# Optimization experiments

Measured on AMD Instinct MI355X. Metric: run time of the kernel, lower is better.

The kernel has to match this reference:

```python
import jax, jax.numpy as jnp
import numpy as np

B, S, HID = 2, 2048, 4096
NH, NKV, HD = 32, 8, 128
MAX_POS = 4096
SCALE = HD ** -0.5


def _rope_tables():
    inv_freq = 1.0 / (10000.0 ** (np.arange(0, HD, 2, dtype=np.float32) / HD))
    t = np.arange(MAX_POS, dtype=np.float32)
    freqs = np.outer(t, inv_freq)              # [MAX_POS, HD/2]
    emb = np.concatenate([freqs, freqs], axis=-1)  # [MAX_POS, HD]
    return jnp.asarray(np.cos(emb)), jnp.asarray(np.sin(emb))


def setup_inputs() -> dict:
    key = jax.random.key(0)
    ks = jax.random.split(key, 6)
    hidden_states = jax.random.normal(ks[0], (B, S, HID), dtype=jnp.float32)
    position_ids = jnp.broadcast_to(jnp.arange(S, dtype=jnp.int64 if jax.config.jax_enable_x64 else jnp.int32), (B, S))
    cos_table, sin_table = _rope_tables()
    # weights stored [in, out] for x @ W
    sd = HID ** -0.5
    Wq = jax.random.normal(ks[1], (HID, NH * HD), dtype=jnp.float32) * sd
    Wk = jax.random.normal(ks[2], (HID, NKV * HD), dtype=jnp.float32) * sd
    Wv = jax.random.normal(ks[3], (HID, NKV * HD), dtype=jnp.float32) * sd
    Wo = jax.random.normal(ks[4], (NH * HD, HID), dtype=jnp.float32) * sd
    return {"hidden_states": hidden_states, "position_ids": position_ids,
            "cos_table": cos_table, "sin_table": sin_table,
            "Wq": Wq, "Wk": Wk, "Wv": Wv, "Wo": Wo}


def _rotate_half(x):
    x1, x2 = jnp.split(x, 2, axis=-1)
    return jnp.concatenate([-x2, x1], axis=-1)


def reference(hidden_states, position_ids, cos_table, sin_table, Wq, Wk, Wv, Wo):
    b, s, _ = hidden_states.shape
    q = (hidden_states @ Wq).reshape(b, s, NH, HD)
    k = (hidden_states @ Wk).reshape(b, s, NKV, HD)
    v = (hidden_states @ Wv).reshape(b, s, NKV, HD)

    # RoPE, cos/sin gathered by position and unsqueezed at head dim (dim=2, bsnd)
    cos = cos_table[position_ids][:, :, None, :]  # [b, s, 1, hd]
    sin = sin_table[position_ids][:, :, None, :]
    q = q * cos + _rotate_half(q) * sin
    k = k * cos + _rotate_half(k) * sin

    # GQA: expand kv heads to match query heads
    rep = NH // NKV
    k = jnp.repeat(k, rep, axis=2)  # [b, s, NH, hd]
    v = jnp.repeat(v, rep, axis=2)

    scores = jnp.einsum('bqnd,bknd->bnqk', q, k) * SCALE  # [b, NH, s, s]
    causal = jnp.tril(jnp.ones((s, s), dtype=bool))
    scores = jnp.where(causal, scores, jnp.finfo(scores.dtype).min)
    probs = jax.nn.softmax(scores, axis=-1)
    attn = jnp.einsum('bnqk,bknd->bqnd', probs, v)  # [b, s, NH, hd]
    attn = attn.reshape(b, s, NH * HD)
    return attn @ Wo
```

## Files before the change

### kernel.cpp

```cpp
#include <hip/hip_runtime.h>
#include <stdint.h>

typedef unsigned short u16;
typedef __bf16 bf16x8 __attribute__((ext_vector_type(8)));
typedef unsigned short u16x8 __attribute__((ext_vector_type(8)));
typedef unsigned short u16x4 __attribute__((ext_vector_type(4)));
typedef float f32x4 __attribute__((ext_vector_type(4)));

#define B_ 2
#define S_ 2048
#define HID_ 4096
#define NH_ 32
#define NKV_ 8
#define HD_ 128
#define NTOT_ 6144
#define SCALE_ 0.08838834764831845f

#define GLD16(gp, lp)                                                     \
  __builtin_amdgcn_global_load_lds(                                       \
      (__attribute__((address_space(1))) void*)(gp),                      \
      (__attribute__((address_space(3))) void*)(lp), 16, 0, 0)

#define BAR __builtin_amdgcn_s_barrier()
#define PRIO1 __builtin_amdgcn_s_setprio(1)
#define PRIO0 __builtin_amdgcn_s_setprio(0)
#define VM8 asm volatile("s_waitcnt vmcnt(8)" ::: "memory")
#define VM0 asm volatile("s_waitcnt vmcnt(0)" ::: "memory")

__device__ __forceinline__ u16 f2b(float f) {
  union { float f; uint32_t u; } v; v.f = f;
  uint32_t u = v.u;
  u = u + 0x7fffu + ((u >> 16) & 1u);
  return (u16)(u >> 16);
}
__device__ __forceinline__ float b2f(u16 s) {
  union { uint32_t u; float f; } v; v.u = ((uint32_t)s) << 16;
  return v.f;
}
__device__ __forceinline__ bf16x8 ldb8(const u16* p) {
  u16x8 u = *(const u16x8*)p;
  return __builtin_bit_cast(bf16x8, u);
}
__device__ __forceinline__ bf16x8 ldb8b(const char* p) {
  u16x8 u = *(const u16x8*)p;
  return __builtin_bit_cast(bf16x8, u);
}

__global__ __launch_bounds__(256) void k_convx(const float* __restrict__ src,
                                               u16* __restrict__ dst, int n4) {
  int i = blockIdx.x * 256 + threadIdx.x;
  if (i >= n4) return;
  const float4 v = ((const float4*)src)[i];
  u16x4 o = { f2b(v.x), f2b(v.y), f2b(v.z), f2b(v.w) };
  *(u16x4*)(dst + (size_t)i * 4) = o;
}

__global__ __launch_bounds__(256) void k_convT(const float* __restrict__ src,
                                               u16* __restrict__ dst, int N, int Kd) {
  __shared__ u16 tile[64][65];
  int k0 = blockIdx.x * 64, n0 = blockIdx.y * 64;
  int t = threadIdx.x;
  int rr = t >> 4;
  int cc = (t & 15) * 4;
#pragma unroll
  for (int p = 0; p < 4; ++p) {
    int r = p * 16 + rr;
    float4 v = *(const float4*)&src[(size_t)(k0 + r) * N + n0 + cc];
    tile[cc + 0][r] = f2b(v.x);
    tile[cc + 1][r] = f2b(v.y);
    tile[cc + 2][r] = f2b(v.z);
    tile[cc + 3][r] = f2b(v.w);
  }
  __syncthreads();
#pragma unroll
  for (int p = 0; p < 4; ++p) {
    int n = p * 16 + rr;
    u16x4 o = { tile[n][cc], tile[n][cc + 1], tile[n][cc + 2], tile[n][cc + 3] };
    *(u16x4*)&dst[(size_t)(n0 + n) * Kd + k0 + cc] = o;
  }
}

__global__ __launch_bounds__(256) void k_convqkv(const float* __restrict__ Wq,
                                                 const float* __restrict__ Wk,
                                                 const float* __restrict__ Wv,
                                                 u16* __restrict__ dst) {
  __shared__ u16 tile[64][65];
  const int Kd = HID_;
  int k0 = blockIdx.x * 64;
  int ng = blockIdx.y * 64;
  const float* src;
  int N, ns;
  if (ng < 4096)      { src = Wq; N = 4096; ns = ng; }
  else if (ng < 5120) { src = Wk; N = 1024; ns = ng - 4096; }
  else                { src = Wv; N = 1024; ns = ng - 5120; }
  int t = threadIdx.x;
  int rr = t >> 4;
  int cc = (t & 15) * 4;
#pragma unroll
  for (int p = 0; p < 4; ++p) {
    int r = p * 16 + rr;
    float4 v = *(const float4*)&src[(size_t)(k0 + r) * N + ns + cc];
    tile[cc + 0][r] = f2b(v.x);
    tile[cc + 1][r] = f2b(v.y);
    tile[cc + 2][r] = f2b(v.z);
    tile[cc + 3][r] = f2b(v.w);
  }
  __syncthreads();
#pragma unroll
  for (int p = 0; p < 4; ++p) {
    int n = p * 16 + rr;
    u16x4 o = { tile[n][cc], tile[n][cc + 1], tile[n][cc + 2], tile[n][cc + 3] };
    *(u16x4*)&dst[(size_t)(ng + n) * Kd + k0 + cc] = o;
  }
}

__global__ __launch_bounds__(512) void k_gemm_out(const u16* __restrict__ A,
                                                  const u16* __restrict__ Bt,
                                                  float* __restrict__ Cf,
                                                  int M, int N, int Kd) {
  __shared__ __align__(16) char smem[131072];
  const int NT = Kd >> 6;

  int nwg = gridDim.x * gridDim.y;
  int orig = blockIdx.y * gridDim.x + blockIdx.x;
  int cpx = nwg >> 3;
  int swz = (orig & 7) * cpx + (orig >> 3);
  int bx = swz % gridDim.x, by = swz / gridDim.x;
  int m0 = by * 256, n0 = bx * 256;

  int t = threadIdx.x, lane = t & 63, wave = t >> 6;
  int wr = wave >> 2, wc = wave & 3;
  int lg = lane >> 4, l16 = lane & 15;
  int loff = l16 * 64 + ((lg ^ ((l16 >> 1) & 3)) << 4);
  int srow = lane >> 2, schk = (lane & 3) ^ ((lane >> 3) & 3);

  const u16* Asrc = A  + (size_t)(m0 + wave * 32 + srow) * Kd + schk * 8;
  const u16* Bsrc = Bt + (size_t)(n0 + wave * 32 + srow) * Kd + schk * 8;

  f32x4 acc[8][4] = {};

#define OST_A(tile, kc, BB) do {                                              \
    char* d_ = smem + (BB) + ((kc) << 14) + (wave << 11);                     \
    const u16* s_ = Asrc + (size_t)(tile) * 64 + (kc) * 32;                   \
    GLD16(s_, d_); GLD16(s_ + (size_t)16 * Kd, d_ + 1024); } while (0)
#define OST_B(tile, kc, BB) do {                                              \
    char* d_ = smem + (BB) + 32768 + ((kc) << 14) + (wave << 11);             \
    const u16* s_ = Bsrc + (size_t)(tile) * 64 + (kc) * 32;                   \
    GLD16(s_, d_); GLD16(s_ + (size_t)16 * Kd, d_ + 1024); } while (0)
#define OLDB(BB, kc) do { _Pragma("unroll")                                   \
    for (int j = 0; j < 4; ++j)                                               \
      bfr[j] = ldb8b(smem + (BB) + 32768 + ((kc) << 14) + ((wc * 4 + j) << 10) + loff); } while (0)
#define OLDA(BB, kc, mh) do { _Pragma("unroll")                               \
    for (int i = 0; i < 4; ++i)                                               \
      af[i] = ldb8b(smem + (BB) + ((kc) << 14) + ((wr * 8 + (mh) * 4 + i) << 10) + loff); } while (0)
#define OMFMA(mh) do { _Pragma("unroll")                                      \
    for (int i = 0; i < 4; ++i) { _Pragma("unroll")                           \
      for (int j = 0; j < 4; ++j)                                             \
        acc[(mh) * 4 + i][j] = __builtin_amdgcn_mfma_f32_16x16x32_bf16(af[i], bfr[j], acc[(mh) * 4 + i][j], 0, 0, 0); } } while (0)

  OST_A(0, 0, 0); OST_B(0, 0, 0); OST_A(0, 1, 0); OST_B(0, 1, 0);
  OST_A(1, 0, 65536); OST_B(1, 0, 65536);
  VM8; BAR;

  for (int it = 0; it < (NT >> 1); ++it) {
    int a = it << 1;
    bool pf = (a + 2 < NT);
    bf16x8 bfr[4], af[4];
    OLDB(0, 0); OLDA(0, 0, 0); OST_A(a + 1, 1, 65536);
    BAR; PRIO1; OMFMA(0); PRIO0; BAR;
    OLDA(0, 0, 1); OST_B(a + 1, 1, 65536);
    BAR; PRIO1; OMFMA(1); PRIO0; if (pf) { VM8; } else { VM0; } BAR;
    OLDB(0, 1); OLDA(0, 1, 0); if (pf) OST_A(a + 2, 0, 0);
    BAR; PRIO1; OMFMA(0); PRIO0; BAR;
    OLDA(0, 1, 1); if (pf) OST_B(a + 2, 0, 0);
    BAR; PRIO1; OMFMA(1); PRIO0; if (pf) { VM8; } else { VM0; } BAR;
    OLDB(65536, 0); OLDA(65536, 0, 0); if (pf) OST_A(a + 2, 1, 0);
    BAR; PRIO1; OMFMA(0); PRIO0; BAR;
    OLDA(65536, 0, 1); if (pf) OST_B(a + 2, 1, 0);
    BAR; PRIO1; OMFMA(1); PRIO0; if (pf) { VM8; } else { VM0; } BAR;
    OLDB(65536, 1); OLDA(65536, 1, 0); if (pf) OST_A(a + 3, 0, 65536);
    BAR; PRIO1; OMFMA(0); PRIO0; BAR;
    OLDA(65536, 1, 1); if (pf) OST_B(a + 3, 0, 65536);
    BAR; PRIO1; OMFMA(1); PRIO0; if (pf) { VM8; } else { VM0; } BAR;
  }
#undef OST_A
#undef OST_B
#undef OLDB
#undef OLDA
#undef OMFMA

#pragma unroll
  for (int i = 0; i < 8; ++i)
#pragma unroll
    for (int j = 0; j < 4; ++j)
#pragma unroll
      for (int r = 0; r < 4; ++r) {
        int m = m0 + wr * 128 + i * 16 + lg * 4 + r;
        int n = n0 + wc * 64 + j * 16 + l16;
        Cf[(size_t)m * N + n] = acc[i][j][r];
      }
}

__global__ __launch_bounds__(512) void k_gqkv(const u16* __restrict__ A,
                                              const u16* __restrict__ Bt,
                                              u16* __restrict__ Qb,
                                              u16* __restrict__ Kb,
                                              u16* __restrict__ Vb) {
  __shared__ __align__(16) char smem[114688];
  const int Kd = HID_;
  const int NT = Kd >> 6;

  int orig = blockIdx.y * 32 + blockIdx.x;
  int swz = (orig & 7) * 64 + (orig >> 3);
  int bx = swz & 31, by = swz >> 5;
  int m0 = by * 256, n0 = bx * 192;

  int t = threadIdx.x, lane = t & 63, wave = t >> 6;
  int wr = wave >> 2, wc = wave & 3;
  int lg = lane >> 4, l16 = lane & 15;
  int loff = l16 * 64 + ((lg ^ ((l16 >> 1) & 3)) << 4);
  int srow = lane >> 2, schk = (lane & 3) ^ ((lane >> 3) & 3);

  const u16* Asrc = A + (size_t)(m0 + wave * 32 + srow) * Kd + schk * 8;
  const u16* sB0 = Bt + (size_t)(n0 + wave * 16 + srow) * Kd + schk * 8;
  const u16* sB1 = Bt + (size_t)(n0 + 128 + (wave & 3) * 16 + srow) * Kd + schk * 8;
  int bdst2 = (8 + (wave & 3)) << 10;

  f32x4 acc[8][3] = {};

#define QST_A(tile, kc, BB) do {                                              \
    char* d_ = smem + (BB) + ((kc) << 14) + (wave << 11);                     \
    const u16* s_ = Asrc + (size_t)(tile) * 64 + (kc) * 32;                   \
    GLD16(s_, d_); GLD16(s_ + (size_t)16 * Kd, d_ + 1024); } while (0)
#define QST_B(tile, kc, BB) do {                                              \
    char* db_ = smem + (BB) + 32768 + (kc) * 12288;                           \
    GLD16(sB0 + (size_t)(tile) * 64 + (kc) * 32, db_ + (wave << 10));         \
    GLD16(sB1 + (size_t)(tile) * 64 + (kc) * 32, db_ + bdst2); } while (0)
#define QLDB(BB, kc) do { _Pragma("unroll")                                   \
    for (int j = 0; j < 3; ++j)                                               \
      bfr[j] = ldb8b(smem + (BB) + 32768 + (kc) * 12288 + ((wc * 3 + j) << 10) + loff); } while (0)
#define QLDA(BB, kc, mh) do { _Pragma("unroll")                               \
    for (int i = 0; i < 4; ++i)                                               \
      af[i] = ldb8b(smem + (BB) + ((kc) << 14) + ((wr * 8 + (mh) * 4 + i) << 10) + loff); } while (0)
#define QMFMA(mh) do { _Pragma("unroll")                                      \
    for (int i = 0; i < 4; ++i) { _Pragma("unroll")                           \
      for (int j = 0; j < 3; ++j)                                             \
        acc[(mh) * 4 + i][j] = __builtin_amdgcn_mfma_f32_16x16x32_bf16(af[i], bfr[j], acc[(mh) * 4 + i][j], 0, 0, 0); } } while (0)

  QST_A(0, 0, 0); QST_B(0, 0, 0); QST_A(0, 1, 0); QST_B(0, 1, 0);
  QST_A(1, 0, 57344); QST_B(1, 0, 57344);
  VM8; BAR;

  for (int it = 0; it < (NT >> 1); ++it) {
    int a = it << 1;
    bool pf = (a + 2 < NT);
    bf16x8 bfr[3], af[4];
    QLDB(0, 0); QLDA(0, 0, 0); QST_A(a + 1, 1, 57344);
    BAR; PRIO1; QMFMA(0); PRIO0; BAR;
    QLDA(0, 0, 1); QST_B(a + 1, 1, 57344);
    BAR; PRIO1; QMFMA(1); PRIO0; if (pf) { VM8; } else { VM0; } BAR;
    QLDB(0, 1); QLDA(0, 1, 0); if (pf) QST_A(a + 2, 0, 0);
    BAR; PRIO1; QMFMA(0); PRIO0; BAR;
    QLDA(0, 1, 1); if (pf) QST_B(a + 2, 0, 0);
    BAR; PRIO1; QMFMA(1); PRIO0; if (pf) { VM8; } else { VM0; } BAR;
    QLDB(57344, 0); QLDA(57344, 0, 0); if (pf) QST_A(a + 2, 1, 0);
    BAR; PRIO1; QMFMA(0); PRIO0; BAR;
    QLDA(57344, 0, 1); if (pf) QST_B(a + 2, 1, 0);
    BAR; PRIO1; QMFMA(1); PRIO0; if (pf) { VM8; } else { VM0; } BAR;
    QLDB(57344, 1); QLDA(57344, 1, 0); if (pf) QST_A(a + 3, 0, 57344);
    BAR; PRIO1; QMFMA(0); PRIO0; BAR;
    QLDA(57344, 1, 1); if (pf) QST_B(a + 3, 0, 57344);
    BAR; PRIO1; QMFMA(1); PRIO0; if (pf) { VM8; } BAR;
  }
#undef QST_A
#undef QST_B
#undef QLDB
#undef QLDA
#undef QMFMA

#pragma unroll
  for (int i = 0; i < 8; ++i)
#pragma unroll
    for (int j = 0; j < 3; ++j)
#pragma unroll
      for (int r = 0; r < 4; ++r) {
        int m = m0 + wr * 128 + i * 16 + lg * 4 + r;
        int n = n0 + wc * 48 + j * 16 + l16;
        int head = n >> 7, d = n & 127;
        int b = m >> 11, s = m & (S_ - 1);
        u16 val = f2b(acc[i][j][r]);
        if (head < NH_) {
          Qb[(((size_t)b * NH_ + head) * S_ + s) * HD_ + d] = val;
        } else if (head < NH_ + NKV_) {
          Kb[(((size_t)b * NKV_ + (head - NH_)) * S_ + s) * HD_ + d] = val;
        } else {
          Vb[(((size_t)b * NKV_ + (head - NH_ - NKV_)) * HD_ + d) * S_ + s] = val;
        }
      }
}

__global__ __launch_bounds__(256) void k_rope2(u16* __restrict__ Qb, u16* __restrict__ Kb,
                                               const int* __restrict__ pos,
                                               const float* __restrict__ ct,
                                               const float* __restrict__ st) {
  int wave = threadIdx.x >> 6, lane = threadIdx.x & 63;
  int row = blockIdx.x * 4 + wave;
  u16* buf;
  int H;
  if (row < B_ * NH_ * S_) { buf = Qb; H = NH_; }
  else { buf = Kb; H = NKV_; row -= B_ * NH_ * S_; }
  int s = row & (S_ - 1);
  int b = row / (H * S_);
  int p = pos[b * S_ + s];
  size_t base = (size_t)row * HD_;
  float x1 = b2f(buf[base + lane]);
  float x2 = b2f(buf[base + 64 + lane]);
  float c  = ct[(size_t)p * HD_ + lane];
  float sn = st[(size_t)p * HD_ + lane];
  buf[base + lane]      = f2b(x1 * c - x2 * sn);
  buf[base + 64 + lane] = f2b(x2 * c + x1 * sn);
}

__global__ __launch_bounds__(256, 4) void k_attn(const u16* __restrict__ Q,
                                                 const u16* __restrict__ K,
                                                 const u16* __restrict__ Vt,
                                                 u16* __restrict__ Ob) {
  __shared__ __align__(16) char smem[40960];
  const int VS_OFF = 16384, PS_OFF = 32768;

  int bid = blockIdx.x;
  int pid = bid & 15;
  int h   = (bid >> 4) & 31;
  int b   = bid >> 9;
  int kvh = h >> 2;
  int tid = threadIdx.x;
  int wave = tid >> 6, lane = tid & 63;
  int lg = lane >> 4, l16 = lane & 15;
  int lsw = (l16 & 7) << 4;

  const u16* Qp = Q  + (((size_t)b * NH_  + h)   * S_) * HD_;
  const u16* Kp = K  + (((size_t)b * NKV_ + kvh) * S_) * HD_;
  const u16* Vp = Vt + (((size_t)b * NKV_ + kvh) * HD_) * S_;

  for (int pass = 0; pass < 2; ++pass) {
    int qt = pass ? (31 - pid) : pid;
    int q0 = qt * 64 + wave * 16;
    int qg = q0 + l16;

    bf16x8 qf[4];
#pragma unroll
    for (int c = 0; c < 4; ++c)
      qf[c] = ldb8(&Qp[(size_t)qg * HD_ + c * 32 + lg * 8]);

    f32x4 oacc[8] = {};
    float mrun = -1e30f, lrun = 0.f;

    int nt = qt + 1;
    for (int tI = 0; tI < nt; ++tI) {
      int kb = tI * 64;
      __syncthreads();
#pragma unroll
      for (int i = 0; i < 4; ++i) {
        int ci = i * 256 + tid;
        int r = ci >> 4, ch = ci & 15;
        u16x8 v = *(const u16x8*)&Kp[(size_t)(kb + r) * HD_ + ch * 8];
        *(u16x8*)(smem + r * 256 + ((ch * 16) ^ ((r & 7) << 4))) = v;
      }
#pragma unroll
      for (int i = 0; i < 4; ++i) {
        int ci = i * 256 + tid;
        int r = ci >> 3, ch = ci & 7;
        u16x8 v = *(const u16x8*)&Vp[(size_t)r * S_ + kb + ch * 8];
        *(u16x8*)(smem + VS_OFF + r * 128 + ((ch * 16) ^ ((r & 7) << 4))) = v;
      }
      __syncthreads();

      f32x4 sc[4] = {};
#pragma unroll
      for (int c = 0; c < 4; ++c) {
#pragma unroll
        for (int n = 0; n < 4; ++n) {
          bf16x8 kf = ldb8b(smem + (n * 16 + l16) * 256 + ((c * 64 + lg * 16) ^ lsw));
          sc[n] = __builtin_amdgcn_mfma_f32_16x16x32_bf16(kf, qf[c], sc[n], 0, 0, 0);
        }
      }

      bool diag = (tI == qt);
      float mx = -1e30f;
#pragma unroll
      for (int n = 0; n < 4; ++n)
#pragma unroll
        for (int r = 0; r < 4; ++r) {
          float v = sc[n][r];
          int key = kb + n * 16 + lg * 4 + r;
          if (diag && key > qg) v = -1e30f;
          sc[n][r] = v;
          mx = fmaxf(mx, v);
        }
      mx = fmaxf(mx, __shfl_xor(mx, 16));
      mx = fmaxf(mx, __shfl_xor(mx, 32));
      float mnew = fmaxf(mrun, mx * SCALE_);
      float alpha = __expf(mrun - mnew);
      float ps = 0.f;
#pragma unroll
      for (int n = 0; n < 4; ++n) {
        u16x4 pk;
#pragma unroll
        for (int r = 0; r < 4; ++r) {
          float p = __expf(fmaf(sc[n][r], SCALE_, -mnew));
          ps += p;
          pk[r] = f2b(p);
        }
        *(u16x4*)(smem + PS_OFF + wave * 2048 + l16 * 128 + ((n * 32 + lg * 8) ^ lsw)) = pk;
      }
      ps += __shfl_xor(ps, 16);
      ps += __shfl_xor(ps, 32);
      lrun = lrun * alpha + ps;
      mrun = mnew;

      float ar[4];
#pragma unroll
      for (int r = 0; r < 4; ++r) ar[r] = __shfl(alpha, lg * 4 + r);
#pragma unroll
      for (int ns = 0; ns < 8; ++ns)
#pragma unroll
        for (int r = 0; r < 4; ++r) oacc[ns][r] *= ar[r];

#pragma unroll
      for (int ck = 0; ck < 2; ++ck) {
        bf16x8 pa = ldb8b(smem + PS_OFF + wave * 2048 + l16 * 128 + ((ck * 64 + lg * 16) ^ lsw));
#pragma unroll
        for (int ns = 0; ns < 8; ++ns) {
          bf16x8 vf = ldb8b(smem + VS_OFF + (ns * 16 + l16) * 128 + ((ck * 64 + lg * 16) ^ lsw));
          oacc[ns] = __builtin_amdgcn_mfma_f32_16x16x32_bf16(pa, vf, oacc[ns], 0, 0, 0);
        }
      }
    }

    float lr[4];
#pragma unroll
    for (int r = 0; r < 4; ++r) lr[r] = 1.0f / __shfl(lrun, lg * 4 + r);
#pragma unroll
    for (int ns = 0; ns < 8; ++ns)
#pragma unroll
      for (int r = 0; r < 4; ++r) {
        int q = q0 + lg * 4 + r;
        Ob[((size_t)(b * S_) + q) * (NH_ * HD_) + h * HD_ + ns * 16 + l16] =
            f2b(oacc[ns][r] * lr[r]);
      }
  }
}

extern "C" void kernel_launch(void* const* d_in, const int* in_sizes, int n_in,
                              void* d_out, int out_size, void* d_ws, size_t ws_size,
                              hipStream_t stream) {
  const float* hs  = (const float*)d_in[0];
  const int*   pos = (const int*)d_in[1];
  const float* ct  = (const float*)d_in[2];
  const float* st  = (const float*)d_in[3];
  const float* Wq  = (const float*)d_in[4];
  const float* Wk  = (const float*)d_in[5];
  const float* Wv  = (const float*)d_in[6];
  const float* Wo  = (const float*)d_in[7];
  float* out = (float*)d_out;

  char* w = (char*)d_ws;
  u16* Xb    = (u16*)(w);
  u16* WqkvT = (u16*)(w + 33554432ull);
  u16* WoT   = (u16*)(w + 83886080ull);
  u16* Qb    = (u16*)(w + 117440512ull);
  u16* Kb    = (u16*)(w + 150994944ull);
  u16* Vb    = (u16*)(w + 159383552ull);
  u16* Attb  = (u16*)(w + 167772160ull);

  k_convx<<<16384, 256, 0, stream>>>(hs, Xb, 4194304);
  k_convqkv<<<dim3(64, 96), 256, 0, stream>>>(Wq, Wk, Wv, WqkvT);
  k_convT<<<dim3(64, 64), 256, 0, stream>>>(Wo, WoT, 4096, 4096);
  k_gqkv<<<dim3(32, 16), 512, 0, stream>>>(Xb, WqkvT, Qb, Kb, Vb);
  k_rope2<<<40960, 256, 0, stream>>>(Qb, Kb, pos, ct, st);
  k_attn<<<1024, 256, 0, stream>>>(Qb, Kb, Vb, Attb);
  k_gemm_out<<<dim3(16, 16), 512, 0, stream>>>(Attb, WoT, out, 4096, 4096, 4096);
}
```

Baseline: 606.1 us.

## Restructure GEMM main loops into register double-buffered LDS pipeline with fewer barriers

Rewrites the K-loop of the output-projection GEMM and the fused QKV GEMM. Each iteration now loads one LDS tile (both k-chunks) into ping-pong register fragment sets X and Y and issues the MFMAs for one set while the other is read from LDS. This cuts barriers from eight to two per 64-wide K tile and tightens the global-load wait from vmcnt(8) to vmcnt(4). It aims to reduce synchronization stalls and overlap LDS reads with MFMA work, at the cost of more live VGPRs for the doubled fragment sets and a shallower global prefetch distance.

```diff
diff --git a/kernel.cpp b/kernel.cpp
--- a/kernel.cpp
+++ b/kernel.cpp
@@ -24,7 +24,7 @@
 #define BAR __builtin_amdgcn_s_barrier()
 #define PRIO1 __builtin_amdgcn_s_setprio(1)
 #define PRIO0 __builtin_amdgcn_s_setprio(0)
-#define VM8 asm volatile("s_waitcnt vmcnt(8)" ::: "memory")
+#define VM4 asm volatile("s_waitcnt vmcnt(4)" ::: "memory")
 #define VM0 asm volatile("s_waitcnt vmcnt(0)" ::: "memory")
 
 __device__ __forceinline__ u16 f2b(float f) {
@@ -139,55 +139,54 @@
 
   f32x4 acc[8][4] = {};
 
-#define OST_A(tile, kc, BB) do {                                              \
-    char* d_ = smem + (BB) + ((kc) << 14) + (wave << 11);                     \
-    const u16* s_ = Asrc + (size_t)(tile) * 64 + (kc) * 32;                   \
-    GLD16(s_, d_); GLD16(s_ + (size_t)16 * Kd, d_ + 1024); } while (0)
-#define OST_B(tile, kc, BB) do {                                              \
-    char* d_ = smem + (BB) + 32768 + ((kc) << 14) + (wave << 11);             \
-    const u16* s_ = Bsrc + (size_t)(tile) * 64 + (kc) * 32;                   \
-    GLD16(s_, d_); GLD16(s_ + (size_t)16 * Kd, d_ + 1024); } while (0)
-#define OLDB(BB, kc) do { _Pragma("unroll")                                   \
+#define OSTG(tile, kc) do {                                                   \
+    int BB_ = ((tile) & 1) << 16;                                             \
+    char* dA_ = smem + BB_ + ((kc) << 14) + (wave << 11);                     \
+    const u16* sA_ = Asrc + (size_t)(tile) * 64 + (kc) * 32;                  \
+    GLD16(sA_, dA_); GLD16(sA_ + (size_t)16 * Kd, dA_ + 1024);                \
+    char* dB_ = smem + BB_ + 32768 + ((kc) << 14) + (wave << 11);             \
+    const u16* sB_ = Bsrc + (size_t)(tile) * 64 + (kc) * 32;                  \
+    GLD16(sB_, dB_); GLD16(sB_ + (size_t)16 * Kd, dB_ + 1024); } while (0)
+#define OREAD(S, bb, kc) do { _Pragma("unroll")                               \
     for (int j = 0; j < 4; ++j)                                               \
-      bfr[j] = ldb8b(smem + (BB) + 32768 + ((kc) << 14) + ((wc * 4 + j) << 10) + loff); } while (0)
-#define OLDA(BB, kc, mh) do { _Pragma("unroll")                               \
+      S##b_[j] = ldb8b(smem + (bb) + 32768 + ((kc) << 14) + ((wc * 4 + j) << 10) + loff); \
+    _Pragma("unroll")                                                         \
     for (int i = 0; i < 4; ++i)                                               \
-      af[i] = ldb8b(smem + (BB) + ((kc) << 14) + ((wr * 8 + (mh) * 4 + i) << 10) + loff); } while (0)
-#define OMFMA(mh) do { _Pragma("unroll")                                      \
+      S##a0[i] = ldb8b(smem + (bb) + ((kc) << 14) + ((wr * 8 + i) << 10) + loff); \
+    _Pragma("unroll")                                                         \
+    for (int i = 0; i < 4; ++i)                                               \
+      S##a1[i] = ldb8b(smem + (bb) + ((kc) << 14) + ((wr * 8 + 4 + i) << 10) + loff); } while (0)
+#define OMM(S) do { PRIO1; _Pragma("unroll")                                  \
     for (int i = 0; i < 4; ++i) { _Pragma("unroll")                           \
       for (int j = 0; j < 4; ++j)                                             \
-        acc[(mh) * 4 + i][j] = __builtin_amdgcn_mfma_f32_16x16x32_bf16(af[i], bfr[j], acc[(mh) * 4 + i][j], 0, 0, 0); } } while (0)
-
-  OST_A(0, 0, 0); OST_B(0, 0, 0); OST_A(0, 1, 0); OST_B(0, 1, 0);
-  OST_A(1, 0, 65536); OST_B(1, 0, 65536);
-  VM8; BAR;
-
-  for (int it = 0; it < (NT >> 1); ++it) {
-    int a = it << 1;
-    bool pf = (a + 2 < NT);
-    bf16x8 bfr[4], af[4];
-    OLDB(0, 0); OLDA(0, 0, 0); OST_A(a + 1, 1, 65536);
-    BAR; PRIO1; OMFMA(0); PRIO0; BAR;
-    OLDA(0, 0, 1); OST_B(a + 1, 1, 65536);
-    BAR; PRIO1; OMFMA(1); PRIO0; if (pf) { VM8; } else { VM0; } BAR;
-    OLDB(0, 1); OLDA(0, 1, 0); if (pf) OST_A(a + 2, 0, 0);
-    BAR; PRIO1; OMFMA(0); PRIO0; BAR;
-    OLDA(0, 1, 1); if (pf) OST_B(a + 2, 0, 0);
-    BAR; PRIO1; OMFMA(1); PRIO0; if (pf) { VM8; } else { VM0; } BAR;
-    OLDB(65536, 0); OLDA(65536, 0, 0); if (pf) OST_A(a + 2, 1, 0);
-    BAR; PRIO1; OMFMA(0); PRIO0; BAR;
-    OLDA(65536, 0, 1); if (pf) OST_B(a + 2, 1, 0);
-    BAR; PRIO1; OMFMA(1); PRIO0; if (pf) { VM8; } else { VM0; } BAR;
-    OLDB(65536, 1); OLDA(65536, 1, 0); if (pf) OST_A(a + 3, 0, 65536);
-    BAR; PRIO1; OMFMA(0); PRIO0; BAR;
-    OLDA(65536, 1, 1); if (pf) OST_B(a + 3, 0, 65536);
-    BAR; PRIO1; OMFMA(1); PRIO0; if (pf) { VM8; } else { VM0; } BAR;
-  }
-#undef OST_A
-#undef OST_B
-#undef OLDB
-#undef OLDA
-#undef OMFMA
+        acc[i][j] = __builtin_amdgcn_mfma_f32_16x16x32_bf16(S##a0[i], S##b_[j], acc[i][j], 0, 0, 0); } \
+    _Pragma("unroll")                                                         \
+    for (int i = 0; i < 4; ++i) { _Pragma("unroll")                           \
+      for (int j = 0; j < 4; ++j)                                             \
+        acc[4 + i][j] = __builtin_amdgcn_mfma_f32_16x16x32_bf16(S##a1[i], S##b_[j], acc[4 + i][j], 0, 0, 0); } \
+    PRIO0; } while (0)
+
+  bf16x8 Xb_[4], Xa0[4], Xa1[4], Yb_[4], Ya0[4], Ya1[4];
+
+  OSTG(0, 0); OSTG(0, 1);
+  VM4; BAR;
+  OREAD(X, 0, 0);
+
+  for (int kt = 0; kt < NT; ++kt) {
+    int bb = (kt & 1) << 16;
+    bool pf = (kt + 1 < NT);
+    if (pf) { OSTG(kt + 1, 0); VM4; } else { VM0; }
+    BAR;
+    OREAD(Y, bb, 1);
+    OMM(X);
+    if (pf) { OSTG(kt + 1, 1); VM4; }
+    BAR;
+    if (pf) OREAD(X, ((kt + 1) & 1) << 16, 0);
+    OMM(Y);
+  }
+#undef OSTG
+#undef OREAD
+#undef OMM
 
 #pragma unroll
   for (int i = 0; i < 8; ++i)
@@ -228,55 +227,54 @@
 
   f32x4 acc[8][3] = {};
 
-#define QST_A(tile, kc, BB) do {                                              \
-    char* d_ = smem + (BB) + ((kc) << 14) + (wave << 11);                     \
-    const u16* s_ = Asrc + (size_t)(tile) * 64 + (kc) * 32;                   \
-    GLD16(s_, d_); GLD16(s_ + (size_t)16 * Kd, d_ + 1024); } while (0)
-#define QST_B(tile, kc, BB) do {                                              \
-    char* db_ = smem + (BB) + 32768 + (kc) * 12288;                           \
-    GLD16(sB0 + (size_t)(tile) * 64 + (kc) * 32, db_ + (wave << 10));         \
-    GLD16(sB1 + (size_t)(tile) * 64 + (kc) * 32, db_ + bdst2); } while (0)
-#define QLDB(BB, kc) do { _Pragma("unroll")                                   \
+#define QSTG(tile, kc) do {                                                   \
+    int BB_ = ((tile) & 1) * 57344;                                           \
+    char* dA_ = smem + BB_ + ((kc) << 14) + (wave << 11);                     \
+    const u16* sA_ = Asrc + (size_t)(tile) * 64 + (kc) * 32;                  \
+    GLD16(sA_, dA_); GLD16(sA_ + (size_t)16 * Kd, dA_ + 1024);                \
+    char* dB_ = smem + BB_ + 32768 + (kc) * 12288;                            \
+    GLD16(sB0 + (size_t)(tile) * 64 + (kc) * 32, dB_ + (wave << 10));         \
+    GLD16(sB1 + (size_t)(tile) * 64 + (kc) * 32, dB_ + bdst2); } while (0)
+#define QREAD(S, bb, kc) do { _Pragma("unroll")                               \
     for (int j = 0; j < 3; ++j)                                               \
-      bfr[j] = ldb8b(smem + (BB) + 32768 + (kc) * 12288 + ((wc * 3 + j) << 10) + loff); } while (0)
-#define QLDA(BB, kc, mh) do { _Pragma("unroll")                               \
+      S##b_[j] = ldb8b(smem + (bb) + 32768 + (kc) * 12288 + ((wc * 3 + j) << 10) + loff); \
+    _Pragma("unroll")                                                         \
     for (int i = 0; i < 4; ++i)                                               \
-      af[i] = ldb8b(smem + (BB) + ((kc) << 14) + ((wr * 8 + (mh) * 4 + i) << 10) + loff); } while (0)
-#define QMFMA(mh) do { _Pragma("unroll")                                      \
+      S##a0[i] = ldb8b(smem + (bb) + ((kc) << 14) + ((wr * 8 + i) << 10) + loff); \
+    _Pragma("unroll")                                                         \
+    for (int i = 0; i < 4; ++i)                                               \
+      S##a1[i] = ldb8b(smem + (bb) + ((kc) << 14) + ((wr * 8 + 4 + i) << 10) + loff); } while (0)
+#define QMM(S) do { PRIO1; _Pragma("unroll")                                  \
     for (int i = 0; i < 4; ++i) { _Pragma("unroll")                           \
       for (int j = 0; j < 3; ++j)                                             \
-        acc[(mh) * 4 + i][j] = __builtin_amdgcn_mfma_f32_16x16x32_bf16(af[i], bfr[j], acc[(mh) * 4 + i][j], 0, 0, 0); } } while (0)
-
-  QST_A(0, 0, 0); QST_B(0, 0, 0); QST_A(0, 1, 0); QST_B(0, 1, 0);
-  QST_A(1, 0, 57344); QST_B(1, 0, 57344);
-  VM8; BAR;
-
-  for (int it = 0; it < (NT >> 1); ++it) {
-    int a = it << 1;
-    bool pf = (a + 2 < NT);
-    bf16x8 bfr[3], af[4];
-    QLDB(0, 0); QLDA(0, 0, 0); QST_A(a + 1, 1, 57344);
-    BAR; PRIO1; QMFMA(0); PRIO0; BAR;
-    QLDA(0, 0, 1); QST_B(a + 1, 1, 57344);
-    BAR; PRIO1; QMFMA(1); PRIO0; if (pf) { VM8; } else { VM0; } BAR;
-    QLDB(0, 1); QLDA(0, 1, 0); if (pf) QST_A(a + 2, 0, 0);
-    BAR; PRIO1; QMFMA(0); PRIO0; BAR;
-    QLDA(0, 1, 1); if (pf) QST_B(a + 2, 0, 0);
-    BAR; PRIO1; QMFMA(1); PRIO0; if (pf) { VM8; } else { VM0; } BAR;
-    QLDB(57344, 0); QLDA(57344, 0, 0); if (pf) QST_A(a + 2, 1, 0);
-    BAR; PRIO1; QMFMA(0); PRIO0; BAR;
-    QLDA(57344, 0, 1); if (pf) QST_B(a + 2, 1, 0);
-    BAR; PRIO1; QMFMA(1); PRIO0; if (pf) { VM8; } else { VM0; } BAR;
-    QLDB(57344, 1); QLDA(57344, 1, 0); if (pf) QST_A(a + 3, 0, 57344);
-    BAR; PRIO1; QMFMA(0); PRIO0; BAR;
-    QLDA(57344, 1, 1); if (pf) QST_B(a + 3, 0, 57344);
-    BAR; PRIO1; QMFMA(1); PRIO0; if (pf) { VM8; } BAR;
-  }
-#undef QST_A
-#undef QST_B
-#undef QLDB
-#undef QLDA
-#undef QMFMA
+        acc[i][j] = __builtin_amdgcn_mfma_f32_16x16x32_bf16(S##a0[i], S##b_[j], acc[i][j], 0, 0, 0); } \
+    _Pragma("unroll")                                                         \
+    for (int i = 0; i < 4; ++i) { _Pragma("unroll")                           \
+      for (int j = 0; j < 3; ++j)                                             \
+        acc[4 + i][j] = __builtin_amdgcn_mfma_f32_16x16x32_bf16(S##a1[i], S##b_[j], acc[4 + i][j], 0, 0, 0); } \
+    PRIO0; } while (0)
+
+  bf16x8 Xb_[3], Xa0[4], Xa1[4], Yb_[3], Ya0[4], Ya1[4];
+
+  QSTG(0, 0); QSTG(0, 1);
+  VM4; BAR;
+  QREAD(X, 0, 0);
+
+  for (int kt = 0; kt < NT; ++kt) {
+    int bb = (kt & 1) * 57344;
+    bool pf = (kt + 1 < NT);
+    if (pf) { QSTG(kt + 1, 0); VM4; } else { VM0; }
+    BAR;
+    QREAD(Y, bb, 1);
+    QMM(X);
+    if (pf) { QSTG(kt + 1, 1); VM4; }
+    BAR;
+    if (pf) QREAD(X, ((kt + 1) & 1) * 57344, 0);
+    QMM(Y);
+  }
+#undef QSTG
+#undef QREAD
+#undef QMM
 
 #pragma unroll
   for (int i = 0; i < 8; ++i)
```

New measurement: 617.5 us. Within noise of the previous version (+1.9%).
